# Performance work log

Hardware: AMD Instinct MI355X
Metric: run time of the kernel (lower is better)

Reference implementation:

```python
import jax, jax.numpy as jnp
import numpy as np

ALPHA = 0.2  # leaky_relu negative slope (init arg `alpha`)
V_NODES = 7

def setup_inputs() -> dict:
    key = jax.random.key(0)
    k1, k2, k3 = jax.random.split(key, 3)
    N, C, T, V = 256, 256, 64, V_NODES
    IN, OUT = C * T, 256
    h = jax.random.normal(k1, (N, C, T, V), dtype=jnp.float32)
    # xavier_uniform with gain=1.414
    limW = 1.414 * np.sqrt(6.0 / (IN + OUT))
    W = jax.random.uniform(k2, (IN, OUT), dtype=jnp.float32, minval=-limW, maxval=limW)
    lima = 1.414 * np.sqrt(6.0 / (2 * OUT + 1))
    a = jax.random.uniform(k3, (2 * OUT, 1), dtype=jnp.float32, minval=-lima, maxval=lima)
    Bp = jnp.zeros((V, V), dtype=jnp.float32)  # torch: zeros(7,7)+1e-6; the 1e-6 is added in reference
    return {"h": h, "W": W, "a": a, "Bp": Bp}

def reference(h, W, a, Bp):
    N, C, T, V = h.shape
    E = W.shape[1]
    # (N,C,T,V) -> (N,V,C*T)
    hf = jnp.transpose(h, (0, 3, 1, 2)).reshape(N, V, C * T)
    Wh = jnp.einsum('nvi,io->nvo', hf, W)  # [N,V,E]
    # pairwise concat score [Wh_i || Wh_j] @ a  ==  Wh_i@a1 + Wh_j@a2 (exact same math, no O(V^2*2E) tensor)
    a1, a2 = a[:E, 0], a[E:, 0]
    s1 = Wh @ a1  # [N,V] (score contribution of row node i)
    s2 = Wh @ a2  # [N,V] (score contribution of col node j)
    e = jax.nn.leaky_relu(s1[:, :, None] + s2[:, None, :], negative_slope=ALPHA)  # [N,V,V]
    attention = jax.nn.softmax(e, axis=-1)
    # learned adjacency: B + I, min-max normalized, sym-normalized D^-1/2 A D^-1/2
    adj = (Bp + 1e-6) + jnp.eye(V, dtype=Bp.dtype)
    adj = (adj - adj.min()) / (adj.max() - adj.min())
    D = jnp.diag(jnp.sum(adj, axis=1))
    D12 = jnp.sqrt(jnp.linalg.inv(D))  # diag -> elementwise sqrt of 1/deg on diagonal
    adj_norm = D12 @ adj @ D12  # [V,V]
    attention = jnp.einsum('ij,njk->nik', adj_norm, attention)  # [N,V,V]
    h_prime = jnp.einsum('nij,njo->nio', attention, Wh)  # [N,V,E]
    return jax.nn.elu(h_prime)
```

## Files before the change

kernel.cpp:

```cpp
#include <hip/hip_runtime.h>
#include <cstdint>

#define KK 16384
#define EE 256
#define M_USED 1792
#define LRELU_ALPHA 0.2f

typedef __bf16 bf16x8 __attribute__((ext_vector_type(8)));
typedef float f32x4 __attribute__((ext_vector_type(4)));

#define WT_BYTES (256u*16384u*2u)

__device__ __forceinline__ unsigned short f2bf(float f){
  union { float f; unsigned u; } x; x.f = f;
  unsigned r = x.u + 0x7fffu + ((x.u >> 16) & 1u);
  return (unsigned short)(r >> 16);
}

__global__ __launch_bounds__(256) void k_transpose_w(const float* __restrict__ W,
                                                     unsigned short* __restrict__ Wt){
  __shared__ float tile[64][65];
  const int i0 = blockIdx.x * 64;
  const int o0 = blockIdx.y * 64;
  const int tid = threadIdx.x;
  #pragma unroll
  for (int r = 0; r < 16; ++r){
    int il = r*4 + (tid >> 6);
    int ol = tid & 63;
    tile[il][ol] = W[(size_t)(i0+il)*EE + o0 + ol];
  }
  __syncthreads();
  #pragma unroll
  for (int r = 0; r < 16; ++r){
    int ol = r*4 + (tid >> 6);
    int il = tid & 63;
    Wt[(size_t)(o0+ol)*KK + i0 + il] = f2bf(tile[il][ol]);
  }
}

__global__ __launch_bounds__(512) void k_gemm(const float* __restrict__ h,
                                              const unsigned short* __restrict__ Wt,
                                              float* __restrict__ part, int planes){
  __shared__ unsigned short Bs[64*72];
  const int tid  = threadIdx.x;
  const int mt   = blockIdx.x;
  const int kc   = blockIdx.y;
  const int n0   = mt * 8;
  const int w    = tid >> 6;
  const int lane = tid & 63;
  const int col  = lane & 15;
  const int quad = lane >> 4;

  for (int idx = tid; idx < 8*72; idx += 512) Bs[56*72 + idx] = 0;

  int hoff[2]; int hlds[2][4]; bool hval[2];
  #pragma unroll
  for (int it = 0; it < 2; ++it){
    int j = tid + it*512;
    hval[it] = (j < 896);
    int jj = hval[it] ? j : 0;
    int nn = jj / 112;
    int f  = jj - nn*112;
    hoff[it] = (n0+nn)*114688 + f*4;
    #pragma unroll
    for (int e = 0; e < 4; ++e){
      int rr = f*4 + e;
      int t_ = rr / 7;
      int v_ = rr - t_*7;
      hlds[it][e] = (nn*7 + v_)*72 + t_;
    }
  }

  const unsigned short* aptr = Wt + (size_t)(w*32 + col)*KK + quad*8;

  f32x4 acc[2][4];
  #pragma unroll
  for (int a_ = 0; a_ < 2; ++a_)
    #pragma unroll
    for (int b_ = 0; b_ < 4; ++b_)
      acc[a_][b_] = (f32x4){0.f, 0.f, 0.f, 0.f};

  const int c0 = kc * planes;
  for (int s = 0; s < planes; ++s){
    const int c = c0 + s;
    {
      const int cb = c*448;
      #pragma unroll
      for (int it = 0; it < 2; ++it){
        if (hval[it]){
          float4 v = *reinterpret_cast<const float4*>(h + (size_t)(hoff[it] + cb));
          Bs[hlds[it][0]] = f2bf(v.x);
          Bs[hlds[it][1]] = f2bf(v.y);
          Bs[hlds[it][2]] = f2bf(v.z);
          Bs[hlds[it][3]] = f2bf(v.w);
        }
      }
    }
    bf16x8 af[2][2];
    #pragma unroll
    for (int oi = 0; oi < 2; ++oi)
      #pragma unroll
      for (int kh = 0; kh < 2; ++kh)
        af[oi][kh] = *reinterpret_cast<const bf16x8*>(aptr + (size_t)oi*16*KK + c*64 + kh*32);
    __syncthreads();
    #pragma unroll
    for (int kh = 0; kh < 2; ++kh){
      bf16x8 bfr[4];
      #pragma unroll
      for (int mi = 0; mi < 4; ++mi)
        bfr[mi] = *reinterpret_cast<const bf16x8*>(&Bs[(mi*16 + col)*72 + kh*32 + quad*8]);
      #pragma unroll
      for (int oi = 0; oi < 2; ++oi)
        #pragma unroll
        for (int mi = 0; mi < 4; ++mi)
          acc[oi][mi] = __builtin_amdgcn_mfma_f32_16x16x32_bf16(af[oi][kh], bfr[mi], acc[oi][mi], 0, 0, 0);
    }
    __syncthreads();
  }

  #pragma unroll
  for (int oi = 0; oi < 2; ++oi){
    #pragma unroll
    for (int r = 0; r < 4; ++r){
      int o = w*32 + oi*16 + quad*4 + r;
      size_t rowbase = ((size_t)(kc*256 + o))*M_USED + mt*56;
      #pragma unroll
      for (int mi = 0; mi < 4; ++mi){
        int ml = mi*16 + col;
        if (ml < 56) part[rowbase + ml] = acc[oi][mi][r];
      }
    }
  }
}

__global__ __launch_bounds__(256) void k_reduce(const float* __restrict__ part,
                                                float* __restrict__ Wh, int nkc){
  const int m = blockIdx.x*256 + threadIdx.x;
  const int o = blockIdx.y;
  float s = 0.f;
  for (int k = 0; k < nkc; ++k)
    s += part[((size_t)(k*256 + o))*M_USED + m];
  Wh[(size_t)o*M_USED + m] = s;
}

__global__ __launch_bounds__(256) void k_attn(const float* __restrict__ Wh,
                                              const float* __restrict__ a,
                                              const float* __restrict__ Bp,
                                              float* __restrict__ out){
  const int n    = blockIdx.x;
  const int tid  = threadIdx.x;
  const int lane = tid & 63;
  const int wv   = tid >> 6;

  __shared__ float adjn[49];
  __shared__ float red1[4][7], red2[4][7];
  __shared__ float s1s[7], s2s[7];
  __shared__ float att0[49], att[49];

  if (tid == 0){
    float adj[49];
    float mn = 1e30f, mx = -1e30f;
    for (int i = 0; i < 7; ++i)
      for (int j = 0; j < 7; ++j){
        float x = Bp[i*7+j] + 1e-6f + (i == j ? 1.f : 0.f);
        adj[i*7+j] = x;
        mn = fminf(mn, x); mx = fmaxf(mx, x);
      }
    float inv = 1.f / (mx - mn);
    for (int i = 0; i < 49; ++i) adj[i] = (adj[i] - mn) * inv;
    float d12[7];
    for (int i = 0; i < 7; ++i){
      float s = 0.f;
      for (int j = 0; j < 7; ++j) s += adj[i*7+j];
      d12[i] = 1.f / sqrtf(s);
    }
    for (int i = 0; i < 7; ++i)
      for (int j = 0; j < 7; ++j)
        adjn[i*7+j] = d12[i] * adj[i*7+j] * d12[j];
  }

  float wh[7];
  #pragma unroll
  for (int v = 0; v < 7; ++v)
    wh[v] = Wh[(size_t)tid*M_USED + n*7 + v];

  const float a1 = a[tid];
  const float a2 = a[256 + tid];

  #pragma unroll
  for (int v = 0; v < 7; ++v){
    float x1 = wh[v]*a1;
    float x2 = wh[v]*a2;
    #pragma unroll
    for (int off = 32; off > 0; off >>= 1){
      x1 += __shfl_down(x1, off);
      x2 += __shfl_down(x2, off);
    }
    if (lane == 0){ red1[wv][v] = x1; red2[wv][v] = x2; }
  }
  __syncthreads();
  if (tid < 7){
    s1s[tid] = red1[0][tid]+red1[1][tid]+red1[2][tid]+red1[3][tid];
    s2s[tid] = red2[0][tid]+red2[1][tid]+red2[2][tid]+red2[3][tid];
  }
  __syncthreads();
  if (tid < 7){
    const int v = tid;
    float e[7]; float mx = -1e30f;
    #pragma unroll
    for (int u = 0; u < 7; ++u){
      float t = s1s[v] + s2s[u];
      t = t > 0.f ? t : LRELU_ALPHA*t;
      e[u] = t; mx = fmaxf(mx, t);
    }
    float sum = 0.f;
    #pragma unroll
    for (int u = 0; u < 7; ++u){ e[u] = expf(e[u]-mx); sum += e[u]; }
    float inv = 1.f/sum;
    #pragma unroll
    for (int u = 0; u < 7; ++u) att0[v*7+u] = e[u]*inv;
  }
  __syncthreads();
  if (tid < 7){
    const int v = tid;
    #pragma unroll
    for (int u = 0; u < 7; ++u){
      float s = 0.f;
      #pragma unroll
      for (int w7 = 0; w7 < 7; ++w7) s += adjn[v*7+w7]*att0[w7*7+u];
      att[v*7+u] = s;
    }
  }
  __syncthreads();
  #pragma unroll
  for (int v = 0; v < 7; ++v){
    float hp = 0.f;
    #pragma unroll
    for (int u = 0; u < 7; ++u) hp += att[v*7+u]*wh[u];
    float o = hp > 0.f ? hp : expm1f(hp);
    out[(size_t)(n*7+v)*256 + tid] = o;
  }
}

extern "C" void kernel_launch(void* const* d_in, const int* in_sizes, int n_in,
                              void* d_out, int out_size, void* d_ws, size_t ws_size,
                              hipStream_t stream){
  const float* h  = (const float*)d_in[0];
  const float* W  = (const float*)d_in[1];
  const float* a  = (const float*)d_in[2];
  const float* Bp = (const float*)d_in[3];
  float* out = (float*)d_out;
  char* ws = (char*)d_ws;

  const size_t part_elems = (size_t)256 * M_USED;
  const size_t need16 = WT_BYTES + (16 + 1) * part_elems * 4;
  const int nkc = (ws_size >= need16) ? 16 : 8;

  unsigned short* Wt   = (unsigned short*)ws;
  float*          part = (float*)(ws + WT_BYTES);
  float*          Wh   = part + (size_t)nkc * part_elems;

  k_transpose_w<<<dim3(256, 4), 256, 0, stream>>>(W, Wt);
  k_gemm<<<dim3(32, nkc), 512, 0, stream>>>(h, Wt, part, 256/nkc);
  k_reduce<<<dim3(7, 256), 256, 0, stream>>>(part, Wh, nkc);
  k_attn<<<256, 256, 0, stream>>>(Wh, a, Bp, out);
}
```

Before: 223.2 us.

## Double-buffer LDS and prefetch h into registers, processing two planes per iteration

The GEMM kernel now handles two channel planes per loop iteration (K=128 per step) using a double-buffered LDS tile. It prefetches the next h planes into registers while the current MFMAs run, and drops the trailing barrier per iteration. The goal is to hide global load latency and halve barrier overhead, at the cost of more registers and more LDS per block. The launch bound of 4 waves per SIMD may cap registers and cause spills.

```diff
diff --git a/kernel.cpp b/kernel.cpp
--- a/kernel.cpp
+++ b/kernel.cpp
@@ -38,10 +38,11 @@
   }
 }
 
-__global__ __launch_bounds__(512) void k_gemm(const float* __restrict__ h,
-                                              const unsigned short* __restrict__ Wt,
-                                              float* __restrict__ part, int planes){
-  __shared__ unsigned short Bs[64*72];
+__global__ __launch_bounds__(512, 4) void k_gemm(const float* __restrict__ h,
+                                                 const unsigned short* __restrict__ Wt,
+                                                 float* __restrict__ part,
+                                                 int cpp ){
+  __shared__ unsigned short Bs[2][64*136];
   const int tid  = threadIdx.x;
   const int mt   = blockIdx.x;
   const int kc   = blockIdx.y;
@@ -51,23 +52,28 @@
   const int col  = lane & 15;
   const int quad = lane >> 4;
 
-  for (int idx = tid; idx < 8*72; idx += 512) Bs[56*72 + idx] = 0;
-
-  int hoff[2]; int hlds[2][4]; bool hval[2];
-  #pragma unroll
-  for (int it = 0; it < 2; ++it){
-    int j = tid + it*512;
-    hval[it] = (j < 896);
-    int jj = hval[it] ? j : 0;
+  for (int idx = tid; idx < 1088; idx += 512){
+    Bs[0][7616 + idx] = 0;
+    Bs[1][7616 + idx] = 0;
+  }
+
+  int ghb[4]; short hlds[4][4];
+  const bool hv3 = (tid < 256);
+  #pragma unroll
+  for (int it = 0; it < 4; ++it){
+    int j  = tid + it*512;
+    if (j >= 1792) j = 0;
+    int p  = j / 896;
+    int jj = j - p*896;
     int nn = jj / 112;
     int f  = jj - nn*112;
-    hoff[it] = (n0+nn)*114688 + f*4;
+    ghb[it] = (n0+nn)*114688 + p*448 + f*4;
     #pragma unroll
     for (int e = 0; e < 4; ++e){
       int rr = f*4 + e;
       int t_ = rr / 7;
       int v_ = rr - t_*7;
-      hlds[it][e] = (nn*7 + v_)*72 + t_;
+      hlds[it][e] = (short)((nn*7 + v_)*136 + p*64 + t_);
     }
   }
 
@@ -80,42 +86,57 @@
     for (int b_ = 0; b_ < 4; ++b_)
       acc[a_][b_] = (f32x4){0.f, 0.f, 0.f, 0.f};
 
-  const int c0 = kc * planes;
-  for (int s = 0; s < planes; ++s){
-    const int c = c0 + s;
-    {
-      const int cb = c*448;
-      #pragma unroll
-      for (int it = 0; it < 2; ++it){
-        if (hval[it]){
-          float4 v = *reinterpret_cast<const float4*>(h + (size_t)(hoff[it] + cb));
-          Bs[hlds[it][0]] = f2bf(v.x);
-          Bs[hlds[it][1]] = f2bf(v.y);
-          Bs[hlds[it][2]] = f2bf(v.z);
-          Bs[hlds[it][3]] = f2bf(v.w);
-        }
+  const int c0    = kc * cpp;
+  const int iters = cpp >> 1;
+
+  float4 hreg[4];
+  {
+    const int cb = c0*448;
+    #pragma unroll
+    for (int it = 0; it < 4; ++it)
+      if (it < 3 || hv3)
+        hreg[it] = *reinterpret_cast<const float4*>(h + (size_t)(ghb[it] + cb));
+  }
+
+  int buf = 0;
+  for (int s = 0; s < iters; ++s){
+    #pragma unroll
+    for (int it = 0; it < 4; ++it){
+      if (it < 3 || hv3){
+        Bs[buf][hlds[it][0]] = f2bf(hreg[it].x);
+        Bs[buf][hlds[it][1]] = f2bf(hreg[it].y);
+        Bs[buf][hlds[it][2]] = f2bf(hreg[it].z);
+        Bs[buf][hlds[it][3]] = f2bf(hreg[it].w);
       }
     }
-    bf16x8 af[2][2];
+    const int kb = (c0 + 2*s)*64;
+    bf16x8 af[2][4];
     #pragma unroll
     for (int oi = 0; oi < 2; ++oi)
       #pragma unroll
-      for (int kh = 0; kh < 2; ++kh)
-        af[oi][kh] = *reinterpret_cast<const bf16x8*>(aptr + (size_t)oi*16*KK + c*64 + kh*32);
+      for (int kh = 0; kh < 4; ++kh)
+        af[oi][kh] = *reinterpret_cast<const bf16x8*>(aptr + (size_t)oi*16*KK + kb + kh*32);
+    if (s + 1 < iters){
+      const int cb = (c0 + 2*(s+1))*448;
+      #pragma unroll
+      for (int it = 0; it < 4; ++it)
+        if (it < 3 || hv3)
+          hreg[it] = *reinterpret_cast<const float4*>(h + (size_t)(ghb[it] + cb));
+    }
     __syncthreads();
     #pragma unroll
-    for (int kh = 0; kh < 2; ++kh){
+    for (int kh = 0; kh < 4; ++kh){
       bf16x8 bfr[4];
       #pragma unroll
       for (int mi = 0; mi < 4; ++mi)
-        bfr[mi] = *reinterpret_cast<const bf16x8*>(&Bs[(mi*16 + col)*72 + kh*32 + quad*8]);
+        bfr[mi] = *reinterpret_cast<const bf16x8*>(&Bs[buf][(mi*16 + col)*136 + kh*32 + quad*8]);
       #pragma unroll
       for (int oi = 0; oi < 2; ++oi)
         #pragma unroll
         for (int mi = 0; mi < 4; ++mi)
           acc[oi][mi] = __builtin_amdgcn_mfma_f32_16x16x32_bf16(af[oi][kh], bfr[mi], acc[oi][mi], 0, 0, 0);
     }
-    __syncthreads();
+    buf ^= 1;
   }
 
   #pragma unroll
```

Result: faster. 216.6 us (-3.0%).

## Pre-pack W and h into MFMA fragment layout, drop LDS staging in GEMM

Applied to the files above, without the earlier changes.

Adds separate pack kernels that convert W and h to bf16 in the exact per-lane MFMA fragment order, so the GEMM loads operands straight from global memory with no LDS and no barriers. The GEMM drops to 256 threads per block, each wave now covering 64 outputs, and register double-buffering hides load latency. The cost is an extra full pass writing and re-reading a bf16 copy of h, which is about 58 MB. The fixed NKC=16 split also drops the earlier check that the workspace is large enough.

```diff
diff --git a/kernel.cpp b/kernel.cpp
--- a/kernel.cpp
+++ b/kernel.cpp
@@ -4,12 +4,19 @@
 #define KK 16384
 #define EE 256
 #define M_USED 1792
+#define NKC 16
 #define LRELU_ALPHA 0.2f
 
 typedef __bf16 bf16x8 __attribute__((ext_vector_type(8)));
 typedef float f32x4 __attribute__((ext_vector_type(4)));
 
-#define WT_BYTES (256u*16384u*2u)
+#define KH_N    512
+#define OG_STR  (KH_N*512)
+#define MG_STR  (KH_N*512)
+#define MT_STR  (4*MG_STR)
+
+#define WP_BYTES (16u*OG_STR*2u)
+#define HP_BYTES (32u*MT_STR*2u)
 
 __device__ __forceinline__ unsigned short f2bf(float f){
   union { float f; unsigned u; } x; x.f = f;
@@ -17,112 +24,132 @@
   return (unsigned short)(r >> 16);
 }
 
-__global__ __launch_bounds__(256) void k_transpose_w(const float* __restrict__ W,
-                                                     unsigned short* __restrict__ Wt){
-  __shared__ float tile[64][65];
-  const int i0 = blockIdx.x * 64;
-  const int o0 = blockIdx.y * 64;
+__global__ __launch_bounds__(256) void k_pack_w(const float* __restrict__ W,
+                                                unsigned short* __restrict__ Wp){
+  __shared__ unsigned short Tw[256*136];
   const int tid = threadIdx.x;
-  #pragma unroll
-  for (int r = 0; r < 16; ++r){
-    int il = r*4 + (tid >> 6);
-    int ol = tid & 63;
-    tile[il][ol] = W[(size_t)(i0+il)*EE + o0 + ol];
-  }
-  __syncthreads();
-  #pragma unroll
-  for (int r = 0; r < 16; ++r){
-    int ol = r*4 + (tid >> 6);
-    int il = tid & 63;
-    Wt[(size_t)(o0+ol)*KK + i0 + il] = f2bf(tile[il][ol]);
-  }
-}
-
-__global__ __launch_bounds__(512) void k_gemm(const float* __restrict__ h,
-                                              const unsigned short* __restrict__ Wt,
-                                              float* __restrict__ part, int planes){
-  __shared__ unsigned short Bs[64*72];
+  const int bk  = blockIdx.x;
+  const int k0  = bk*128;
+  #pragma unroll
+  for (int it = 0; it < 32; ++it){
+    int j   = tid + it*256;
+    int k_l = j >> 6;
+    int o4  = j & 63;
+    float4 v = *reinterpret_cast<const float4*>(W + (size_t)(k0 + k_l)*EE + o4*4);
+    Tw[(o4*4+0)*136 + k_l] = f2bf(v.x);
+    Tw[(o4*4+1)*136 + k_l] = f2bf(v.y);
+    Tw[(o4*4+2)*136 + k_l] = f2bf(v.z);
+    Tw[(o4*4+3)*136 + k_l] = f2bf(v.w);
+  }
+  __syncthreads();
+  const int wv = tid >> 6, lane = tid & 63, col = lane & 15, quad = lane >> 4;
+  #pragma unroll
+  for (int i = 0; i < 16; ++i){
+    int tidx = wv*16 + i;
+    int og = tidx >> 2, kh_l = tidx & 3;
+    bf16x8 v = *reinterpret_cast<const bf16x8*>(&Tw[(og*16 + col)*136 + kh_l*32 + quad*8]);
+    *reinterpret_cast<bf16x8*>(Wp + (size_t)og*OG_STR + (size_t)(bk*4 + kh_l)*512
+                               + col*32 + quad*8) = v;
+  }
+}
+
+__global__ __launch_bounds__(256) void k_pack_h(const float* __restrict__ h,
+                                                unsigned short* __restrict__ Hp){
+  __shared__ unsigned short Tm[64*520];
+  const int tid = threadIdx.x;
+  const int mt  = blockIdx.x;
+  const int cc  = blockIdx.y;
+  const int n0  = mt*8;
+  const int c0  = cc*8;
+  for (int idx = tid; idx < 8*520; idx += 256) Tm[56*520 + idx] = 0;
+  #pragma unroll
+  for (int it = 0; it < 28; ++it){
+    int j  = tid + it*256;
+    int nn = j / 896;
+    int r  = j - nn*896;
+    int ci = r / 112;
+    int f  = r - ci*112;
+    float4 v = *reinterpret_cast<const float4*>(
+        h + (size_t)(n0+nn)*114688 + (size_t)(c0+ci)*448 + f*4);
+    float vv[4] = {v.x, v.y, v.z, v.w};
+    #pragma unroll
+    for (int e = 0; e < 4; ++e){
+      int rr = f*4 + e;
+      int t_ = rr / 7;
+      int v_ = rr - t_*7;
+      Tm[(nn*7 + v_)*520 + ci*64 + t_] = f2bf(vv[e]);
+    }
+  }
+  __syncthreads();
+  const int wv = tid >> 6, lane = tid & 63, col = lane & 15, quad = lane >> 4;
+  #pragma unroll
+  for (int i = 0; i < 16; ++i){
+    int tidx = wv*16 + i;
+    int mg = tidx >> 4, kh_l = tidx & 15;
+    bf16x8 v = *reinterpret_cast<const bf16x8*>(&Tm[(mg*16 + col)*520 + kh_l*32 + quad*8]);
+    *reinterpret_cast<bf16x8*>(Hp + (size_t)mt*MT_STR + (size_t)mg*MG_STR
+                               + (size_t)(cc*16 + kh_l)*512 + col*32 + quad*8) = v;
+  }
+}
+
+__global__ __launch_bounds__(256, 2) void k_gemm(const unsigned short* __restrict__ Wp,
+                                                 const unsigned short* __restrict__ Hp,
+                                                 float* __restrict__ part){
   const int tid  = threadIdx.x;
   const int mt   = blockIdx.x;
   const int kc   = blockIdx.y;
-  const int n0   = mt * 8;
   const int w    = tid >> 6;
   const int lane = tid & 63;
   const int col  = lane & 15;
   const int quad = lane >> 4;
-
-  for (int idx = tid; idx < 8*72; idx += 512) Bs[56*72 + idx] = 0;
-
-  int hoff[2]; int hlds[2][4]; bool hval[2];
-  #pragma unroll
-  for (int it = 0; it < 2; ++it){
-    int j = tid + it*512;
-    hval[it] = (j < 896);
-    int jj = hval[it] ? j : 0;
-    int nn = jj / 112;
-    int f  = jj - nn*112;
-    hoff[it] = (n0+nn)*114688 + f*4;
-    #pragma unroll
-    for (int e = 0; e < 4; ++e){
-      int rr = f*4 + e;
-      int t_ = rr / 7;
-      int v_ = rr - t_*7;
-      hlds[it][e] = (nn*7 + v_)*72 + t_;
-    }
-  }
-
-  const unsigned short* aptr = Wt + (size_t)(w*32 + col)*KK + quad*8;
-
-  f32x4 acc[2][4];
-  #pragma unroll
-  for (int a_ = 0; a_ < 2; ++a_)
+  const int lofs = col*32 + quad*8;
+
+  const unsigned short* A0 = Wp + (size_t)(w*4)*OG_STR + (size_t)(kc*32)*512 + lofs;
+  const unsigned short* B0 = Hp + (size_t)mt*MT_STR   + (size_t)(kc*32)*512 + lofs;
+
+  f32x4 acc[4][4];
+  #pragma unroll
+  for (int a_ = 0; a_ < 4; ++a_)
     #pragma unroll
     for (int b_ = 0; b_ < 4; ++b_)
       acc[a_][b_] = (f32x4){0.f, 0.f, 0.f, 0.f};
 
-  const int c0 = kc * planes;
-  for (int s = 0; s < planes; ++s){
-    const int c = c0 + s;
-    {
-      const int cb = c*448;
-      #pragma unroll
-      for (int it = 0; it < 2; ++it){
-        if (hval[it]){
-          float4 v = *reinterpret_cast<const float4*>(h + (size_t)(hoff[it] + cb));
-          Bs[hlds[it][0]] = f2bf(v.x);
-          Bs[hlds[it][1]] = f2bf(v.y);
-          Bs[hlds[it][2]] = f2bf(v.z);
-          Bs[hlds[it][3]] = f2bf(v.w);
-        }
-      }
-    }
-    bf16x8 af[2][2];
-    #pragma unroll
-    for (int oi = 0; oi < 2; ++oi)
-      #pragma unroll
-      for (int kh = 0; kh < 2; ++kh)
-        af[oi][kh] = *reinterpret_cast<const bf16x8*>(aptr + (size_t)oi*16*KK + c*64 + kh*32);
-    __syncthreads();
-    #pragma unroll
-    for (int kh = 0; kh < 2; ++kh){
-      bf16x8 bfr[4];
+  bf16x8 a0[4], b0[4], a1[4], b1[4];
+  #pragma unroll
+  for (int i = 0; i < 4; ++i){
+    a0[i] = *reinterpret_cast<const bf16x8*>(A0 + (size_t)i*OG_STR);
+    b0[i] = *reinterpret_cast<const bf16x8*>(B0 + (size_t)i*MG_STR);
+  }
+
+  for (int s = 0; s < 32; s += 2){
+    #pragma unroll
+    for (int i = 0; i < 4; ++i){
+      a1[i] = *reinterpret_cast<const bf16x8*>(A0 + (size_t)i*OG_STR + (s+1)*512);
+      b1[i] = *reinterpret_cast<const bf16x8*>(B0 + (size_t)i*MG_STR + (s+1)*512);
+    }
+    #pragma unroll
+    for (int oi = 0; oi < 4; ++oi)
       #pragma unroll
       for (int mi = 0; mi < 4; ++mi)
-        bfr[mi] = *reinterpret_cast<const bf16x8*>(&Bs[(mi*16 + col)*72 + kh*32 + quad*8]);
-      #pragma unroll
-      for (int oi = 0; oi < 2; ++oi)
-        #pragma unroll
-        for (int mi = 0; mi < 4; ++mi)
-          acc[oi][mi] = __builtin_amdgcn_mfma_f32_16x16x32_bf16(af[oi][kh], bfr[mi], acc[oi][mi], 0, 0, 0);
-    }
-    __syncthreads();
-  }
-
-  #pragma unroll
-  for (int oi = 0; oi < 2; ++oi){
+        acc[oi][mi] = __builtin_amdgcn_mfma_f32_16x16x32_bf16(a0[oi], b0[mi], acc[oi][mi], 0, 0, 0);
+    const int sn = (s+2 < 32) ? s+2 : 30;
+    #pragma unroll
+    for (int i = 0; i < 4; ++i){
+      a0[i] = *reinterpret_cast<const bf16x8*>(A0 + (size_t)i*OG_STR + sn*512);
+      b0[i] = *reinterpret_cast<const bf16x8*>(B0 + (size_t)i*MG_STR + sn*512);
+    }
+    #pragma unroll
+    for (int oi = 0; oi < 4; ++oi)
+      #pragma unroll
+      for (int mi = 0; mi < 4; ++mi)
+        acc[oi][mi] = __builtin_amdgcn_mfma_f32_16x16x32_bf16(a1[oi], b1[mi], acc[oi][mi], 0, 0, 0);
+  }
+
+  #pragma unroll
+  for (int oi = 0; oi < 4; ++oi){
     #pragma unroll
     for (int r = 0; r < 4; ++r){
-      int o = w*32 + oi*16 + quad*4 + r;
+      int o = (w*4 + oi)*16 + quad*4 + r;
       size_t rowbase = ((size_t)(kc*256 + o))*M_USED + mt*56;
       #pragma unroll
       for (int mi = 0; mi < 4; ++mi){
@@ -134,11 +161,12 @@
 }
 
 __global__ __launch_bounds__(256) void k_reduce(const float* __restrict__ part,
-                                                float* __restrict__ Wh, int nkc){
+                                                float* __restrict__ Wh){
   const int m = blockIdx.x*256 + threadIdx.x;
   const int o = blockIdx.y;
   float s = 0.f;
-  for (int k = 0; k < nkc; ++k)
+  #pragma unroll
+  for (int k = 0; k < NKC; ++k)
     s += part[((size_t)(k*256 + o))*M_USED + m];
   Wh[(size_t)o*M_USED + m] = s;
 }
@@ -252,16 +280,14 @@
   float* out = (float*)d_out;
   char* ws = (char*)d_ws;
 
-  const size_t part_elems = (size_t)256 * M_USED;
-  const size_t need16 = WT_BYTES + (16 + 1) * part_elems * 4;
-  const int nkc = (ws_size >= need16) ? 16 : 8;
-
-  unsigned short* Wt   = (unsigned short*)ws;
-  float*          part = (float*)(ws + WT_BYTES);
-  float*          Wh   = part + (size_t)nkc * part_elems;
-
-  k_transpose_w<<<dim3(256, 4), 256, 0, stream>>>(W, Wt);
-  k_gemm<<<dim3(32, nkc), 512, 0, stream>>>(h, Wt, part, 256/nkc);
-  k_reduce<<<dim3(7, 256), 256, 0, stream>>>(part, Wh, nkc);
+  unsigned short* Wp   = (unsigned short*)ws;
+  unsigned short* Hp   = (unsigned short*)(ws + WP_BYTES);
+  float*          part = (float*)(ws + WP_BYTES + HP_BYTES);
+  float*          Wh   = part + (size_t)NKC * 256 * M_USED;
+
+  k_pack_w<<<128, 256, 0, stream>>>(W, Wp);
+  k_pack_h<<<dim3(32, 32), 256, 0, stream>>>(h, Hp);
+  k_gemm<<<dim3(32, NKC), 256, 0, stream>>>(Wp, Hp, part);
+  k_reduce<<<dim3(7, 256), 256, 0, stream>>>(part, Wh);
   k_attn<<<256, 256, 0, stream>>>(Wh, a, Bp, out);
 }
```

New measurement: 263.7 us. 18.1% more time.
